# Kernel optimization log

Hardware: AMD Instinct MI355X
Metric: run time of the kernel (lower is better)

The kernel has to match this reference:

```python
import jax, jax.numpy as jnp
import numpy as np

N_NODES = 50000
N_EDGES = 800000
N_GRAPHS = 64


def graph_conv(x, edge_index, w_rel, b_rel, w_root):
    # PyG GraphConv with aggr='add':
    #   out = lin_rel(sum_{j in N(i)} x_j) + lin_root(x_i)
    src, dst = edge_index[0], edge_index[1]
    agg = jax.ops.segment_sum(x[src], dst, num_segments=x.shape[0])  # [N, d_in]
    return agg @ w_rel + b_rel + x @ w_root  # [N, d_out]


def scatter_mean(x, batch, num_segments):
    s = jax.ops.segment_sum(x, batch, num_segments=num_segments)
    cnt = jax.ops.segment_sum(jnp.ones((x.shape[0],), x.dtype), batch,
                              num_segments=num_segments)
    return s / jnp.maximum(cnt, 1.0)[:, None]


def setup_inputs() -> dict:
    key = jax.random.key(0)
    ks = jax.random.split(key, 8)
    d_feat, d_hid, d_out = 128, 128, 128
    x = jax.random.normal(ks[0], (N_NODES, d_feat), dtype=jnp.float32)
    edge_index = jax.random.randint(ks[1], (2, N_EDGES), 0, N_NODES, dtype=jnp.int64)
    batch = jnp.sort(jax.random.randint(ks[2], (N_NODES,), 0, N_GRAPHS, dtype=jnp.int64))

    def glorot(k, shape):
        fan_in = shape[0]
        return jax.random.normal(k, shape, dtype=jnp.float32) / np.sqrt(fan_in)

    return {
        "x": x,
        "edge_index": edge_index,
        "batch": batch,
        "w_rel1": glorot(ks[3], (d_feat, d_hid)),
        "b_rel1": jnp.zeros((d_hid,), jnp.float32),
        "w_root1": glorot(ks[4], (d_feat, d_hid)),
        "w_rel2": glorot(ks[5], (d_hid, 2 * d_hid)),
        "b_rel2": jnp.zeros((2 * d_hid,), jnp.float32),
        "w_root2": glorot(ks[6], (d_hid, 2 * d_hid)),
        "w_rel3": glorot(ks[7], (2 * d_hid, d_out)),
        "b_rel3": jnp.zeros((d_out,), jnp.float32),
        "w_root3": glorot(jax.random.fold_in(key, 99), (2 * d_hid, d_out)),
    }


def reference(x, edge_index, batch,
              w_rel1, b_rel1, w_root1,
              w_rel2, b_rel2, w_root2,
              w_rel3, b_rel3, w_root3):
    h = jax.nn.elu(graph_conv(x, edge_index, w_rel1, b_rel1, w_root1))
    h = jax.nn.elu(graph_conv(h, edge_index, w_rel2, b_rel2, w_root2))
    h = jax.nn.elu(graph_conv(h, edge_index, w_rel3, b_rel3, w_root3))
    return scatter_mean(h, batch, N_GRAPHS)  # [num_graphs, n_out]
```

## Files before the change

kernel.cpp:

```cpp
#include <hip/hip_runtime.h>
#include <math.h>

#define NN 50000
#define NNP 50048
#define NE 800000
#define NG 64
#define NBK 196
#define ECH 4082
#define TOTH (NBK * NBK)
#define NBH 151

typedef __attribute__((ext_vector_type(8))) __bf16 bf16x8;
typedef __attribute__((ext_vector_type(8))) short short8;
typedef __attribute__((ext_vector_type(4))) float f32x4;

__device__ inline unsigned short f2bf(float f) {
    unsigned int u = __float_as_uint(f);
    u += 0x7fffu + ((u >> 16) & 1u);
    return (unsigned short)(u >> 16);
}
__device__ inline float bflo(unsigned int v) { return __uint_as_float(v << 16); }
__device__ inline float bfhi(unsigned int v) { return __uint_as_float(v & 0xffff0000u); }
__device__ inline float bfs(unsigned short v) { return __uint_as_float((unsigned int)v << 16); }

#define GLD_LDS16(g, l)                                                          \
    __builtin_amdgcn_global_load_lds(                                            \
        (const __attribute__((address_space(1))) unsigned int*)(g),              \
        (__attribute__((address_space(3))) unsigned int*)(l), 16, 0, 0)

__global__ __launch_bounds__(256) void setup_k(const float* __restrict__ x,
                                               const float* __restrict__ wr1,
                                               const float* __restrict__ wo1,
                                               const float* __restrict__ wr2,
                                               const float* __restrict__ wo2,
                                               const float* __restrict__ wr3,
                                               const float* __restrict__ wo3,
                                               unsigned short* __restrict__ xb,
                                               unsigned short* __restrict__ W1T,
                                               unsigned short* __restrict__ W2T,
                                               unsigned short* __restrict__ W3T) {
    int id = blockIdx.x * 256 + threadIdx.x;
    if (id < NN * 32) {
        float4 v = ((const float4*)x)[id];
        unsigned int p0 = ((unsigned int)f2bf(v.y) << 16) | f2bf(v.x);
        unsigned int p1 = ((unsigned int)f2bf(v.w) << 16) | f2bf(v.z);
        ((uint2*)xb)[id] = make_uint2(p0, p1);
        return;
    }
    int w = id - NN * 32;
    if (w < 32768) {
        int n = w >> 8, k = w & 255;
        W1T[w] = f2bf((k < 128) ? wr1[k * 128 + n] : wo1[(k - 128) * 128 + n]);
    } else if (w < 98304) {
        int j = w - 32768; int n = j >> 8, k = j & 255;
        W2T[j] = f2bf((k < 128) ? wr2[k * 256 + n] : wo2[(k - 128) * 256 + n]);
    } else if (w < 163840) {
        int j = w - 98304; int n = j >> 8, k = j & 255;
        W3T[j] = f2bf((n < 128) ? wr3[k * 128 + n] : wo3[k * 128 + (n - 128)]);
    }
}

__global__ __launch_bounds__(256) void hist_k(const int* __restrict__ dst,
                                              int* __restrict__ H) {
    __shared__ int h[NBK];
    int t = threadIdx.x, k = blockIdx.x;
    if (t < NBK) h[t] = 0;
    __syncthreads();
    int e0 = k * ECH, e1 = min(NE, e0 + ECH);
    for (int e = e0 + t; e < e1; e += 256) atomicAdd(&h[dst[e] >> 8], 1);
    __syncthreads();
    if (t < NBK) H[t * NBK + k] = h[t];
}

__global__ __launch_bounds__(256) void hsum_k(const int* __restrict__ H,
                                              int* __restrict__ hb) {
    int i = blockIdx.x * 256 + threadIdx.x;
    int v = (i < TOTH) ? H[i] : 0;
    for (int off = 32; off; off >>= 1) v += __shfl_xor(v, off, 64);
    __shared__ int ws[4];
    if ((threadIdx.x & 63) == 0) ws[threadIdx.x >> 6] = v;
    __syncthreads();
    if (threadIdx.x == 0) hb[blockIdx.x] = ws[0] + ws[1] + ws[2] + ws[3];
}

__global__ __launch_bounds__(256) void hscan_k(const int* __restrict__ hb,
                                               int* __restrict__ hoff) {
    __shared__ int s[256];
    int t = threadIdx.x;
    int v = (t < NBH) ? hb[t] : 0;
    s[t] = v; __syncthreads();
    for (int off = 1; off < 256; off <<= 1) {
        int u = (t >= off) ? s[t - off] : 0;
        __syncthreads(); s[t] += u; __syncthreads();
    }
    hoff[t] = (t == 0) ? 0 : s[t - 1];
}

__global__ __launch_bounds__(256) void happly_k(const int* __restrict__ H,
                                                const int* __restrict__ hoff,
                                                int* __restrict__ S) {
    int t = threadIdx.x;
    int i = blockIdx.x * 256 + t;
    int v = (i < TOTH) ? H[i] : 0;
    __shared__ int s[256];
    s[t] = v; __syncthreads();
    for (int off = 1; off < 256; off <<= 1) {
        int u = (t >= off) ? s[t - off] : 0;
        __syncthreads(); s[t] += u; __syncthreads();
    }
    if (i < TOTH) S[i] = hoff[blockIdx.x] + s[t] - v;
}

__global__ __launch_bounds__(256) void scatter_k(const int* __restrict__ src,
                                                 const int* __restrict__ dst,
                                                 const int* __restrict__ S,
                                                 int* __restrict__ tmp) {
    __shared__ int cur[NBK];
    int t = threadIdx.x, k = blockIdx.x;
    if (t < NBK) cur[t] = S[t * NBK + k];
    __syncthreads();
    int e0 = k * ECH, e1 = min(NE, e0 + ECH);
    for (int e = e0 + t; e < e1; e += 256) {
        int d = dst[e];
        int p = atomicAdd(&cur[d >> 8], 1);
        tmp[p] = ((d & 255) << 16) | src[e];
    }
}

__global__ __launch_bounds__(256) void csr_k(const int* __restrict__ tmp,
                                             const int* __restrict__ S,
                                             int* __restrict__ rowptr,
                                             int* __restrict__ colsrc) {
    __shared__ int hist[256], off[256], cur[256];
    int t = threadIdx.x, b = blockIdx.x;
    int base = S[b * NBK];
    int next = (b < NBK - 1) ? S[(b + 1) * NBK] : NE;
    int cntb = next - base;
    hist[t] = 0;
    __syncthreads();
    for (int i = t; i < cntb; i += 256) atomicAdd(&hist[tmp[base + i] >> 16], 1);
    __syncthreads();
    int v = hist[t];
    off[t] = v; __syncthreads();
    for (int o = 1; o < 256; o <<= 1) {
        int u = (t >= o) ? off[t - o] : 0;
        __syncthreads(); off[t] += u; __syncthreads();
    }
    int excl = off[t] - v;
    int node = b * 256 + t;
    if (node <= NN) rowptr[node] = base + excl;
    cur[t] = excl;
    __syncthreads();
    for (int i = t; i < cntb; i += 256) {
        int e = tmp[base + i];
        int p = atomicAdd(&cur[e >> 16], 1);
        colsrc[base + p] = e & 0xffff;
    }
}

__global__ __launch_bounds__(256) void aggb_k(const unsigned short* __restrict__ feat,
                                              const int* __restrict__ rowptr,
                                              const int* __restrict__ colsrc,
                                              unsigned short* __restrict__ outp) {
    int node = __builtin_amdgcn_readfirstlane((int)(blockIdx.x * 4 + (threadIdx.x >> 6)));
    int lane = threadIdx.x & 63;
    int beg = rowptr[node], end = rowptr[node + 1];
    float ax = 0.f, ay = 0.f;
    int e = beg;
    for (; e + 4 <= end; e += 4) {
        int s0 = colsrc[e], s1 = colsrc[e + 1], s2 = colsrc[e + 2], s3 = colsrc[e + 3];
        unsigned int v0 = *(const unsigned int*)&feat[(size_t)s0 * 128 + lane * 2];
        unsigned int v1 = *(const unsigned int*)&feat[(size_t)s1 * 128 + lane * 2];
        unsigned int v2 = *(const unsigned int*)&feat[(size_t)s2 * 128 + lane * 2];
        unsigned int v3 = *(const unsigned int*)&feat[(size_t)s3 * 128 + lane * 2];
        ax += bflo(v0); ay += bfhi(v0);
        ax += bflo(v1); ay += bfhi(v1);
        ax += bflo(v2); ay += bfhi(v2);
        ax += bflo(v3); ay += bfhi(v3);
    }
    for (; e < end; ++e) {
        unsigned int v0 = *(const unsigned int*)&feat[(size_t)colsrc[e] * 128 + lane * 2];
        ax += bflo(v0); ay += bfhi(v0);
    }
    unsigned int p = ((unsigned int)f2bf(ay) << 16) | f2bf(ax);
    *(unsigned int*)&outp[(size_t)node * 128 + lane * 2] = p;
}

__global__ __launch_bounds__(256) void aggf_k(const unsigned short* __restrict__ y,
                                              const unsigned short* __restrict__ rr,
                                              const float* __restrict__ b3,
                                              const int* __restrict__ rowptr,
                                              const int* __restrict__ colsrc,
                                              unsigned short* __restrict__ outp) {
    int node = __builtin_amdgcn_readfirstlane((int)(blockIdx.x * 4 + (threadIdx.x >> 6)));
    int lane = threadIdx.x & 63;
    int beg = rowptr[node], end = rowptr[node + 1];
    float ax = 0.f, ay = 0.f;
    int e = beg;
    for (; e + 4 <= end; e += 4) {
        int s0 = colsrc[e], s1 = colsrc[e + 1], s2 = colsrc[e + 2], s3 = colsrc[e + 3];
        unsigned int v0 = *(const unsigned int*)&y[(size_t)s0 * 128 + lane * 2];
        unsigned int v1 = *(const unsigned int*)&y[(size_t)s1 * 128 + lane * 2];
        unsigned int v2 = *(const unsigned int*)&y[(size_t)s2 * 128 + lane * 2];
        unsigned int v3 = *(const unsigned int*)&y[(size_t)s3 * 128 + lane * 2];
        ax += bflo(v0); ay += bfhi(v0);
        ax += bflo(v1); ay += bfhi(v1);
        ax += bflo(v2); ay += bfhi(v2);
        ax += bflo(v3); ay += bfhi(v3);
    }
    for (; e < end; ++e) {
        unsigned int v0 = *(const unsigned int*)&y[(size_t)colsrc[e] * 128 + lane * 2];
        ax += bflo(v0); ay += bfhi(v0);
    }
    unsigned int rv = *(const unsigned int*)&rr[(size_t)node * 128 + lane * 2];
    float2 bb = *(const float2*)&b3[lane * 2];
    float vx = ax + bflo(rv) + bb.x;
    float vy = ay + bfhi(rv) + bb.y;
    vx = vx > 0.f ? vx : (__expf(vx) - 1.f);
    vy = vy > 0.f ? vy : (__expf(vy) - 1.f);
    unsigned int p = ((unsigned int)f2bf(vy) << 16) | f2bf(vx);
    *(unsigned int*)&outp[(size_t)node * 128 + lane * 2] = p;
}

template <int MT, int KA, int N, bool TWO, bool BIAS, bool ELU, bool SPLIT>
__global__ __launch_bounds__(256) void gemm_k(const unsigned short* __restrict__ A1,
                                              const unsigned short* __restrict__ A2,
                                              const unsigned short* __restrict__ WT,
                                              const float* __restrict__ bias,
                                              unsigned short* __restrict__ Cout,
                                              unsigned short* __restrict__ Cout2) {
    constexpr int KTOT = TWO ? 2 * KA : KA;
    constexpr int MI = MT / 32;
    __shared__ __attribute__((aligned(16))) unsigned short As[MT * 32];
    __shared__ __attribute__((aligned(16))) unsigned short Bs[128 * 32];
    const int t = threadIdx.x;
    const int wv = t >> 6, lane = t & 63;
    const int qd = lane >> 4, l16 = lane & 15;
    const int m0 = blockIdx.x * MT, n0 = blockIdx.y * 128;
    const int mh = (wv & 1) * (MT / 2), nh = (wv >> 1) * 64;
    const int srow = lane >> 2;
    const int skk  = (lane & 3) * 8;

    f32x4 acc[MI][4] = {};

    for (int k0 = 0; k0 < KTOT; k0 += 32) {
        const unsigned short* Abase = (TWO && k0 >= KA) ? (A2 + (k0 - KA)) : (A1 + k0);
#pragma unroll
        for (int i = 0; i < MT / 64; ++i) {
            int chunk = wv * (MT / 64) + i;
            const unsigned short* g = Abase + (size_t)(m0 + chunk * 16 + srow) * KA + skk;
            GLD_LDS16(g, &As[chunk * 512]);
        }
        const unsigned short* Wbase = WT + k0;
#pragma unroll
        for (int i = 0; i < 2; ++i) {
            int chunk = wv * 2 + i;
            const unsigned short* g = Wbase + (size_t)(n0 + chunk * 16 + srow) * KTOT + skk;
            GLD_LDS16(g, &Bs[chunk * 512]);
        }
        __syncthreads();
        bf16x8 af[MI], bfr[4];
#pragma unroll
        for (int mi = 0; mi < MI; ++mi)
            af[mi] = *(const bf16x8*)&As[(mh + mi * 16 + l16) * 32 + qd * 8];
#pragma unroll
        for (int ni = 0; ni < 4; ++ni)
            bfr[ni] = *(const bf16x8*)&Bs[(nh + ni * 16 + l16) * 32 + qd * 8];
#pragma unroll
        for (int mi = 0; mi < MI; ++mi)
#pragma unroll
            for (int ni = 0; ni < 4; ++ni)
                acc[mi][ni] = __builtin_amdgcn_mfma_f32_16x16x32_bf16(
                    af[mi], bfr[ni], acc[mi][ni], 0, 0, 0);
        __syncthreads();
    }

#pragma unroll
    for (int mi = 0; mi < MI; ++mi) {
#pragma unroll
        for (int ni = 0; ni < 4; ++ni) {
#pragma unroll
            for (int r = 0; r < 4; ++r) {
                int mm = m0 + mh + mi * 16 + qd * 4 + r;
                if (mm < NN) {
                    int nn = n0 + nh + ni * 16 + l16;
                    float v = acc[mi][ni][r];
                    if (BIAS) v += bias[nn];
                    if (ELU) v = v > 0.f ? v : (__expf(v) - 1.f);
                    unsigned short b = f2bf(v);
                    if (SPLIT) {
                        unsigned short* dst = (nn < 128) ? Cout : Cout2;
                        dst[(size_t)mm * 128 + (nn & 127)] = b;
                    } else {
                        Cout[(size_t)mm * N + nn] = b;
                    }
                }
            }
        }
    }
}

__global__ __launch_bounds__(128) void bounds_k(const int* __restrict__ batch,
                                                int* __restrict__ bounds,
                                                float* __restrict__ outp) {
    int g = threadIdx.x;
    if (g <= NG) {
        int lo = 0, hi = NN;
        while (lo < hi) {
            int mid = (lo + hi) >> 1;
            if (batch[mid] < g) lo = mid + 1; else hi = mid;
        }
        bounds[g] = lo;
    }
    for (int i = threadIdx.x; i < NG * 128; i += 128) outp[i] = 0.f;
}

__global__ __launch_bounds__(128) void sum_k(const unsigned short* __restrict__ vals,
                                             const int* __restrict__ batch,
                                             float* __restrict__ outsum) {
    const int CH = 25;
    int n0 = blockIdx.x * CH;
    int c = threadIdx.x;
    int g = batch[n0];
    float acc = 0.f;
    for (int i = 0; i < CH; ++i) {
        int n = n0 + i;
        int gn = batch[n];
        if (gn != g) {
            unsafeAtomicAdd(&outsum[(size_t)g * 128 + c], acc);
            acc = 0.f; g = gn;
        }
        acc += bfs(vals[(size_t)n * 128 + c]);
    }
    unsafeAtomicAdd(&outsum[(size_t)g * 128 + c], acc);
}

__global__ void divide_k(const int* __restrict__ bounds, float* __restrict__ out) {
    int i = blockIdx.x * 256 + threadIdx.x;
    if (i < NG * 128) {
        int g = i >> 7;
        float c = (float)(bounds[g + 1] - bounds[g]);
        out[i] /= fmaxf(c, 1.f);
    }
}

extern "C" void kernel_launch(void* const* d_in, const int* in_sizes, int n_in,
                              void* d_out, int out_size, void* d_ws, size_t ws_size,
                              hipStream_t stream) {
    const float* x       = (const float*)d_in[0];
    const int*   ei      = (const int*)d_in[1];
    const int*   batch   = (const int*)d_in[2];
    const float* w_rel1  = (const float*)d_in[3];
    const float* b_rel1  = (const float*)d_in[4];
    const float* w_root1 = (const float*)d_in[5];
    const float* w_rel2  = (const float*)d_in[6];
    const float* b_rel2  = (const float*)d_in[7];
    const float* w_root2 = (const float*)d_in[8];
    const float* w_rel3  = (const float*)d_in[9];
    const float* b_rel3  = (const float*)d_in[10];
    const float* w_root3 = (const float*)d_in[11];
    const int* esrc = ei;
    const int* edst = ei + NE;

    unsigned short* Ab = (unsigned short*)d_ws;
    unsigned short* Bb = Ab + (size_t)NNP * 128;
    unsigned short* Cb = Bb + (size_t)NNP * 128;
    unsigned short* xb = Cb + (size_t)NNP * 256;
    unsigned short* W1T = xb + (size_t)NNP * 128;
    unsigned short* W2T = W1T + 128 * 256;
    unsigned short* W3T = W2T + 256 * 256;
    int* rowptr = (int*)(W3T + 256 * 256);
    int* colsrc = rowptr + (NN + 1);
    int* tmp    = colsrc + NE;
    int* H      = tmp + NE;
    int* S      = H + TOTH;
    int* hb     = S + TOTH;
    int* hoff   = hb + 256;
    int* bounds = hoff + 256;
    float* outp = (float*)d_out;

    setup_k<<<(NN * 32 + 163840 + 255) / 256, 256, 0, stream>>>(
        x, w_rel1, w_root1, w_rel2, w_root2, w_rel3, w_root3, xb, W1T, W2T, W3T);
    hist_k<<<NBK, 256, 0, stream>>>(edst, H);
    hsum_k<<<NBH, 256, 0, stream>>>(H, hb);
    hscan_k<<<1, 256, 0, stream>>>(hb, hoff);
    happly_k<<<NBH, 256, 0, stream>>>(H, hoff, S);
    scatter_k<<<NBK, 256, 0, stream>>>(esrc, edst, S, tmp);
    csr_k<<<NBK, 256, 0, stream>>>(tmp, S, rowptr, colsrc);
    bounds_k<<<1, 128, 0, stream>>>(batch, bounds, outp);

    aggb_k<<<NN / 4, 256, 0, stream>>>(xb, rowptr, colsrc, Ab);
    gemm_k<64, 128, 128, true, true, true, false>
        <<<dim3(NNP / 64, 1), 256, 0, stream>>>(Ab, xb, W1T, b_rel1, Bb, nullptr);

    aggb_k<<<NN / 4, 256, 0, stream>>>(Bb, rowptr, colsrc, Ab);
    gemm_k<128, 128, 256, true, true, true, false>
        <<<dim3(NNP / 128, 2), 256, 0, stream>>>(Ab, Bb, W2T, b_rel2, Cb, nullptr);

    gemm_k<128, 256, 256, false, false, false, true>
        <<<dim3(NNP / 128, 2), 256, 0, stream>>>(Cb, nullptr, W3T, nullptr, Ab, Bb);

    aggf_k<<<NN / 4, 256, 0, stream>>>(Ab, Bb, b_rel3, rowptr, colsrc, Cb);
    sum_k<<<NN / 25, 128, 0, stream>>>(Cb, batch, outp);
    divide_k<<<(NG * 128 + 255) / 256, 256, 0, stream>>>(bounds, outp);
}
```

Before: 308.4 us.

## Use full-width 64x256 GEMM tiles for N=256 layers and deepen gather unroll

Adds a gemm256_k kernel where each block computes a 64-row by full-256-column output tile, so the A tile is loaded once instead of once per 128-column half. This replaces the 2-D grid launches for layers 2 and 3 and removes redundant A-matrix traffic. The neighbor-gather loops in the aggregation kernels now unroll 8 edges instead of 4, putting more independent loads in flight. The cost is more registers and LDS per block in the new GEMM, which may lower occupancy.

```diff
diff --git a/kernel.cpp b/kernel.cpp
--- a/kernel.cpp
+++ b/kernel.cpp
@@ -11,7 +11,6 @@
 #define NBH 151
 
 typedef __attribute__((ext_vector_type(8))) __bf16 bf16x8;
-typedef __attribute__((ext_vector_type(8))) short short8;
 typedef __attribute__((ext_vector_type(4))) float f32x4;
 
 __device__ inline unsigned short f2bf(float f) {
@@ -167,16 +166,13 @@
     int beg = rowptr[node], end = rowptr[node + 1];
     float ax = 0.f, ay = 0.f;
     int e = beg;
-    for (; e + 4 <= end; e += 4) {
-        int s0 = colsrc[e], s1 = colsrc[e + 1], s2 = colsrc[e + 2], s3 = colsrc[e + 3];
-        unsigned int v0 = *(const unsigned int*)&feat[(size_t)s0 * 128 + lane * 2];
-        unsigned int v1 = *(const unsigned int*)&feat[(size_t)s1 * 128 + lane * 2];
-        unsigned int v2 = *(const unsigned int*)&feat[(size_t)s2 * 128 + lane * 2];
-        unsigned int v3 = *(const unsigned int*)&feat[(size_t)s3 * 128 + lane * 2];
-        ax += bflo(v0); ay += bfhi(v0);
-        ax += bflo(v1); ay += bfhi(v1);
-        ax += bflo(v2); ay += bfhi(v2);
-        ax += bflo(v3); ay += bfhi(v3);
+    for (; e + 8 <= end; e += 8) {
+        unsigned int v[8];
+#pragma unroll
+        for (int i = 0; i < 8; ++i)
+            v[i] = *(const unsigned int*)&feat[(size_t)colsrc[e + i] * 128 + lane * 2];
+#pragma unroll
+        for (int i = 0; i < 8; ++i) { ax += bflo(v[i]); ay += bfhi(v[i]); }
     }
     for (; e < end; ++e) {
         unsigned int v0 = *(const unsigned int*)&feat[(size_t)colsrc[e] * 128 + lane * 2];
@@ -197,16 +193,13 @@
     int beg = rowptr[node], end = rowptr[node + 1];
     float ax = 0.f, ay = 0.f;
     int e = beg;
-    for (; e + 4 <= end; e += 4) {
-        int s0 = colsrc[e], s1 = colsrc[e + 1], s2 = colsrc[e + 2], s3 = colsrc[e + 3];
-        unsigned int v0 = *(const unsigned int*)&y[(size_t)s0 * 128 + lane * 2];
-        unsigned int v1 = *(const unsigned int*)&y[(size_t)s1 * 128 + lane * 2];
-        unsigned int v2 = *(const unsigned int*)&y[(size_t)s2 * 128 + lane * 2];
-        unsigned int v3 = *(const unsigned int*)&y[(size_t)s3 * 128 + lane * 2];
-        ax += bflo(v0); ay += bfhi(v0);
-        ax += bflo(v1); ay += bfhi(v1);
-        ax += bflo(v2); ay += bfhi(v2);
-        ax += bflo(v3); ay += bfhi(v3);
+    for (; e + 8 <= end; e += 8) {
+        unsigned int v[8];
+#pragma unroll
+        for (int i = 0; i < 8; ++i)
+            v[i] = *(const unsigned int*)&y[(size_t)colsrc[e + i] * 128 + lane * 2];
+#pragma unroll
+        for (int i = 0; i < 8; ++i) { ax += bflo(v[i]); ay += bfhi(v[i]); }
     }
     for (; e < end; ++e) {
         unsigned int v0 = *(const unsigned int*)&y[(size_t)colsrc[e] * 128 + lane * 2];
@@ -222,13 +215,12 @@
     *(unsigned int*)&outp[(size_t)node * 128 + lane * 2] = p;
 }
 
-template <int MT, int KA, int N, bool TWO, bool BIAS, bool ELU, bool SPLIT>
+template <int MT, int KA, int N, bool TWO, bool BIAS, bool ELU>
 __global__ __launch_bounds__(256) void gemm_k(const unsigned short* __restrict__ A1,
                                               const unsigned short* __restrict__ A2,
                                               const unsigned short* __restrict__ WT,
                                               const float* __restrict__ bias,
-                                              unsigned short* __restrict__ Cout,
-                                              unsigned short* __restrict__ Cout2) {
+                                              unsigned short* __restrict__ Cout) {
     constexpr int KTOT = TWO ? 2 * KA : KA;
     constexpr int MI = MT / 32;
     __shared__ __attribute__((aligned(16))) unsigned short As[MT * 32];
@@ -236,7 +228,7 @@
     const int t = threadIdx.x;
     const int wv = t >> 6, lane = t & 63;
     const int qd = lane >> 4, l16 = lane & 15;
-    const int m0 = blockIdx.x * MT, n0 = blockIdx.y * 128;
+    const int m0 = blockIdx.x * MT, n0 = 0;
     const int mh = (wv & 1) * (MT / 2), nh = (wv >> 1) * 64;
     const int srow = lane >> 2;
     const int skk  = (lane & 3) * 8;
@@ -276,14 +268,80 @@
     }
 
 #pragma unroll
-    for (int mi = 0; mi < MI; ++mi) {
-#pragma unroll
-        for (int ni = 0; ni < 4; ++ni) {
+    for (int mi = 0; mi < MI; ++mi)
+#pragma unroll
+        for (int ni = 0; ni < 4; ++ni)
 #pragma unroll
             for (int r = 0; r < 4; ++r) {
                 int mm = m0 + mh + mi * 16 + qd * 4 + r;
                 if (mm < NN) {
                     int nn = n0 + nh + ni * 16 + l16;
+                    float v = acc[mi][ni][r];
+                    if (BIAS) v += bias[nn];
+                    if (ELU) v = v > 0.f ? v : (__expf(v) - 1.f);
+                    Cout[(size_t)mm * N + nn] = f2bf(v);
+                }
+            }
+}
+
+template <int KA, bool TWO, bool BIAS, bool ELU, bool SPLIT>
+__global__ __launch_bounds__(256) void gemm256_k(const unsigned short* __restrict__ A1,
+                                                 const unsigned short* __restrict__ A2,
+                                                 const unsigned short* __restrict__ WT,
+                                                 const float* __restrict__ bias,
+                                                 unsigned short* __restrict__ Cout,
+                                                 unsigned short* __restrict__ Cout2) {
+    constexpr int KTOT = TWO ? 2 * KA : KA;
+    __shared__ __attribute__((aligned(16))) unsigned short As[64 * 32];
+    __shared__ __attribute__((aligned(16))) unsigned short Bs[256 * 32];
+    const int t = threadIdx.x;
+    const int wv = t >> 6, lane = t & 63;
+    const int qd = lane >> 4, l16 = lane & 15;
+    const int m0 = blockIdx.x * 64;
+    const int srow = lane >> 2;
+    const int skk  = (lane & 3) * 8;
+
+    f32x4 acc[4][4] = {};
+
+    for (int k0 = 0; k0 < KTOT; k0 += 32) {
+        const unsigned short* Abase = (TWO && k0 >= KA) ? (A2 + (k0 - KA)) : (A1 + k0);
+        {
+            const unsigned short* g = Abase + (size_t)(m0 + wv * 16 + srow) * KA + skk;
+            GLD_LDS16(g, &As[wv * 512]);
+        }
+        const unsigned short* Wbase = WT + k0;
+#pragma unroll
+        for (int i = 0; i < 4; ++i) {
+            int chunk = wv * 4 + i;
+            const unsigned short* g = Wbase + (size_t)(chunk * 16 + srow) * KTOT + skk;
+            GLD_LDS16(g, &Bs[chunk * 512]);
+        }
+        __syncthreads();
+        bf16x8 af[4], bfr[4];
+#pragma unroll
+        for (int mi = 0; mi < 4; ++mi)
+            af[mi] = *(const bf16x8*)&As[(mi * 16 + l16) * 32 + qd * 8];
+#pragma unroll
+        for (int ni = 0; ni < 4; ++ni)
+            bfr[ni] = *(const bf16x8*)&Bs[(wv * 64 + ni * 16 + l16) * 32 + qd * 8];
+#pragma unroll
+        for (int mi = 0; mi < 4; ++mi)
+#pragma unroll
+            for (int ni = 0; ni < 4; ++ni)
+                acc[mi][ni] = __builtin_amdgcn_mfma_f32_16x16x32_bf16(
+                    af[mi], bfr[ni], acc[mi][ni], 0, 0, 0);
+        __syncthreads();
+    }
+
+#pragma unroll
+    for (int mi = 0; mi < 4; ++mi)
+#pragma unroll
+        for (int ni = 0; ni < 4; ++ni)
+#pragma unroll
+            for (int r = 0; r < 4; ++r) {
+                int mm = m0 + mi * 16 + qd * 4 + r;
+                if (mm < NN) {
+                    int nn = wv * 64 + ni * 16 + l16;
                     float v = acc[mi][ni][r];
                     if (BIAS) v += bias[nn];
                     if (ELU) v = v > 0.f ? v : (__expf(v) - 1.f);
@@ -292,12 +350,10 @@
                         unsigned short* dst = (nn < 128) ? Cout : Cout2;
                         dst[(size_t)mm * 128 + (nn & 127)] = b;
                     } else {
-                        Cout[(size_t)mm * N + nn] = b;
+                        Cout[(size_t)mm * 256 + nn] = b;
                     }
                 }
             }
-        }
-    }
 }
 
 __global__ __launch_bounds__(128) void bounds_k(const int* __restrict__ batch,
@@ -390,15 +446,15 @@
     bounds_k<<<1, 128, 0, stream>>>(batch, bounds, outp);
 
     aggb_k<<<NN / 4, 256, 0, stream>>>(xb, rowptr, colsrc, Ab);
-    gemm_k<64, 128, 128, true, true, true, false>
-        <<<dim3(NNP / 64, 1), 256, 0, stream>>>(Ab, xb, W1T, b_rel1, Bb, nullptr);
+    gemm_k<64, 128, 128, true, true, true>
+        <<<NNP / 64, 256, 0, stream>>>(Ab, xb, W1T, b_rel1, Bb);
 
     aggb_k<<<NN / 4, 256, 0, stream>>>(Bb, rowptr, colsrc, Ab);
-    gemm_k<128, 128, 256, true, true, true, false>
-        <<<dim3(NNP / 128, 2), 256, 0, stream>>>(Ab, Bb, W2T, b_rel2, Cb, nullptr);
-
-    gemm_k<128, 256, 256, false, false, false, true>
-        <<<dim3(NNP / 128, 2), 256, 0, stream>>>(Cb, nullptr, W3T, nullptr, Ab, Bb);
+    gemm256_k<128, true, true, true, false>
+        <<<NNP / 64, 256, 0, stream>>>(Ab, Bb, W2T, b_rel2, Cb, nullptr);
+
+    gemm256_k<256, false, false, false, true>
+        <<<NNP / 64, 256, 0, stream>>>(Cb, nullptr, W3T, nullptr, Ab, Bb);
 
     aggf_k<<<NN / 4, 256, 0, stream>>>(Ab, Bb, b_rel3, rowptr, colsrc, Cb);
     sum_k<<<NN / 25, 128, 0, stream>>>(Cb, batch, outp);
```

Measured after the change: 308.7 us. No clear change (+0.1%).
